# Performance work log

Hardware: AMD Instinct MI355X
Metric: run time of the kernel (lower is better)

The kernel has to match this reference:

```python
import jax, jax.numpy as jnp
import numpy as np

N, E, F_IN, HID, L, G, FFN = 100000, 1600000, 64, 128, 4, 512, 300
BN_EPS = 1e-5


def setup_inputs() -> dict:
    key = jax.random.key(0)
    ks = jax.random.split(key, 16)
    s = 0.05
    inp = {}
    inp["x"] = jax.random.normal(ks[0], (N, F_IN), dtype=jnp.float32)
    inp["edge_index"] = jax.random.randint(ks[1], (2, E), 0, N)
    inp["batch"] = jnp.sort(jax.random.randint(ks[2], (N,), 0, G))
    inp["enc_W"] = jax.random.normal(ks[3], (F_IN, HID), dtype=jnp.float32) * s
    inp["enc_b"] = jnp.zeros((HID,), jnp.float32)
    inp["Ws"] = jax.random.normal(ks[4], (L, HID, HID), dtype=jnp.float32) * s
    inp["bs"] = jnp.zeros((L, HID), jnp.float32)
    inp["bn_gamma"] = jnp.ones((L, HID), jnp.float32)
    inp["bn_beta"] = jnp.zeros((L, HID), jnp.float32)
    inp["bn_mean"] = jax.random.normal(ks[5], (L, HID), dtype=jnp.float32) * 0.01
    inp["bn_var"] = jnp.ones((L, HID), jnp.float32)
    inp["mlp_W0"] = jax.random.normal(ks[6], (HID, FFN), dtype=jnp.float32) * s
    inp["mlp_b0"] = jnp.zeros((FFN,), jnp.float32)
    inp["mlp_W1"] = jax.random.normal(ks[7], (FFN, FFN), dtype=jnp.float32) * s
    inp["mlp_b1"] = jnp.zeros((FFN,), jnp.float32)
    inp["mlp_W2"] = jax.random.normal(ks[8], (FFN, 1), dtype=jnp.float32) * s
    inp["mlp_b2"] = jnp.zeros((1,), jnp.float32)
    return inp


def reference(x, edge_index, batch, enc_W, enc_b, Ws, bs, bn_gamma, bn_beta,
              bn_mean, bn_var, mlp_W0, mlp_b0, mlp_W1, mlp_b1, mlp_W2, mlp_b2):
    # --- GCN normalization with self-loops (constant wrt params) ---
    loop = jnp.arange(N)
    row = jnp.concatenate([edge_index[0], loop])  # source
    col = jnp.concatenate([edge_index[1], loop])  # target (aggregation)
    deg = jax.ops.segment_sum(jnp.ones((E + N,), jnp.float32), col, num_segments=N)
    dinv = jnp.where(deg > 0, jax.lax.rsqrt(deg), 0.0)
    norm = dinv[row] * dinv[col]  # [E+N]

    # node encoder
    h = x @ enc_W + enc_b  # [N, HID]

    for i in range(L):
        h_prev = h
        # GCNConv: D^-1/2 (A+I) D^-1/2 (h W) + b
        hw = h @ Ws[i]
        msg = norm[:, None] * hw[row]                      # [E+N, HID]
        h = jax.ops.segment_sum(msg, col, num_segments=N) + bs[i]
        # BatchNorm1d (eval mode, running stats)
        h = (h - bn_mean[i]) * jax.lax.rsqrt(bn_var[i] + BN_EPS) * bn_gamma[i] + bn_beta[i]
        h = jax.nn.relu(h)
        if i > 0:
            h = h + h_prev

    # global mean pool over graphs
    sums = jax.ops.segment_sum(h, batch, num_segments=G)   # [G, HID]
    cnts = jax.ops.segment_sum(jnp.ones((N,), jnp.float32), batch, num_segments=G)
    gfeat = sums / jnp.maximum(cnts, 1.0)[:, None]

    # output MLP
    o = jax.nn.relu(gfeat @ mlp_W0 + mlp_b0)
    o = jax.nn.relu(o @ mlp_W1 + mlp_b1)
    return o @ mlp_W2 + mlp_b2  # [G, 1]
```

## Files before the change

kernel.cpp:

```cpp
#include <hip/hip_runtime.h>
#include <hip/hip_fp16.h>

#define NN 100000
#define NE 1600000
#define FIN 64
#define HID 128
#define NL 4
#define NG 512
#define FFN 300
#define BN_EPS 1e-5f
#define LDH 136
#define NB 512
#define NPB 196
#define CURPAD 16

static inline size_t alignup(size_t x) { return (x + 255) & ~(size_t)255; }

struct half8 { __half2 h[4]; };

typedef _Float16 f16;
typedef __attribute__((ext_vector_type(4))) _Float16 f16x4;
typedef __attribute__((ext_vector_type(8))) _Float16 f16x8;
typedef __attribute__((ext_vector_type(4))) float f32x4;

__global__ __launch_bounds__(1024) void k_bcount(const int* __restrict__ col,
                                                 int* __restrict__ bcnt) {
    __shared__ int h[NB];
    int t = threadIdx.x;
    if (t < NB) h[t] = 0;
    __syncthreads();
    for (int e = blockIdx.x * 1024 + t; e < NE; e += 256 * 1024)
        atomicAdd(&h[col[e] / NPB], 1);
    __syncthreads();
    if (t < NB && h[t] > 0) atomicAdd(&bcnt[t], h[t]);
}

__global__ void k_bscan(const int* __restrict__ bcnt, int* __restrict__ bbase,
                        int* __restrict__ bcur) {
    __shared__ int s[NB];
    int t = threadIdx.x;
    int v = bcnt[t];
    s[t] = v;
    __syncthreads();
    for (int off = 1; off < NB; off <<= 1) {
        int u = (t >= off) ? s[t - off] : 0;
        __syncthreads();
        s[t] += u;
        __syncthreads();
    }
    int excl = s[t] - v;
    bbase[t] = excl;
    bcur[t * CURPAD] = excl;
    if (t == NB - 1) bbase[NB] = s[t];
}

__global__ __launch_bounds__(1024) void k_bscatter2(const int* __restrict__ row,
                                                    const int* __restrict__ col,
                                                    int* __restrict__ bcur,
                                                    int* __restrict__ ebuf) {
    __shared__ int hcnt[NB];
    __shared__ int hbase[NB];
    int t = threadIdx.x;
    int e0 = blockIdx.x * 4096;
    if (t < NB) hcnt[t] = 0;
    __syncthreads();
    #pragma unroll
    for (int k = 0; k < 4; ++k) {
        int e = e0 + k * 1024 + t;
        if (e < NE) atomicAdd(&hcnt[col[e] / NPB], 1);
    }
    __syncthreads();
    if (t < NB) {
        int c = hcnt[t];
        hbase[t] = (c > 0) ? atomicAdd(&bcur[t * CURPAD], c) : 0;
    }
    __syncthreads();
    if (t < NB) hcnt[t] = 0;
    __syncthreads();
    #pragma unroll
    for (int k = 0; k < 4; ++k) {
        int e = e0 + k * 1024 + t;
        if (e < NE) {
            int c = col[e];
            int b = c / NPB;
            int loc = atomicAdd(&hcnt[b], 1);
            ebuf[hbase[b] + loc] = row[e] | ((c - b * NPB) << 17);
        }
    }
}

__global__ __launch_bounds__(256) void k_binfill(const int* __restrict__ ebuf,
                                                 const int* __restrict__ bbase,
                                                 int* __restrict__ offs,
                                                 int* __restrict__ ends,
                                                 float* __restrict__ dinv,
                                                 int* __restrict__ csr_src) {
    __shared__ int cnt[NPB];
    __shared__ int scn[256];
    __shared__ int cur[NPB];
    int b = blockIdx.x, t = threadIdx.x;
    int lo = b * NPB;
    int hi = lo + NPB; if (hi > NN) hi = NN;
    int n = hi - lo;
    if (n <= 0) return;
    int s0 = bbase[b], s1 = bbase[b + 1];
    for (int i = t; i < NPB; i += 256) cnt[i] = 0;
    __syncthreads();
    for (int j = s0 + t; j < s1; j += 256)
        atomicAdd(&cnt[((unsigned)ebuf[j]) >> 17], 1);
    __syncthreads();
    int v = (t < n) ? cnt[t] : 0;
    scn[t] = v;
    __syncthreads();
    for (int off = 1; off < 256; off <<= 1) {
        int u = (t >= off) ? scn[t - off] : 0;
        __syncthreads();
        scn[t] += u;
        __syncthreads();
    }
    if (t < n) {
        int g = s0 + scn[t] - v;
        offs[lo + t] = g;
        ends[lo + t] = g + v;
        dinv[lo + t] = rsqrtf((float)(v + 1));
        cur[t] = g;
    }
    __syncthreads();
    for (int j = s0 + t; j < s1; j += 256) {
        int e = ebuf[j];
        int pos = atomicAdd(&cur[((unsigned)e) >> 17], 1);
        csr_src[pos] = e & 0x1FFFF;
    }
}

__global__ void k_convW(const float* __restrict__ Ws, const float* __restrict__ encW,
                        f16* __restrict__ wt, f16* __restrict__ wte) {
    int tid = blockIdx.x * 256 + threadIdx.x;
    for (int i = tid; i < NL * HID * HID; i += 64 * 256) {
        int l = i >> 14, rem = i & 16383;
        int c = rem >> 7, k = rem & 127;
        wt[i] = (f16)Ws[(l << 14) + k * HID + c];
    }
    for (int i = tid; i < HID * FIN; i += 64 * 256) {
        int c = i >> 6, k = i & 63;
        wte[i] = (f16)encW[k * HID + c];
    }
}

__global__ __launch_bounds__(256) void k_enc_mfma(const float* __restrict__ x,
                                                  const f16* __restrict__ wte,
                                                  const float* __restrict__ b,
                                                  __half* __restrict__ h) {
    __shared__ f16 sx[64 * 72];
    __shared__ f16 sw[128 * 72];
    int t = threadIdx.x;
    int row0 = blockIdx.x * 64;
    for (int idx = t; idx < 64 * 16; idx += 256) {
        int r = idx >> 4, c4 = (idx & 15) * 4;
        float4 v = {0.0f, 0.0f, 0.0f, 0.0f};
        if (row0 + r < NN) v = *(const float4*)(x + (size_t)(row0 + r) * FIN + c4);
        f16x4 o = {(f16)v.x, (f16)v.y, (f16)v.z, (f16)v.w};
        *(f16x4*)&sx[r * 72 + c4] = o;
    }
    for (int idx = t; idx < 128 * 8; idx += 256) {
        int c = idx >> 3, ch = (idx & 7) * 8;
        *(f16x8*)&sw[c * 72 + ch] = *(const f16x8*)(wte + c * FIN + ch);
    }
    __syncthreads();
    int w = t >> 6, lane = t & 63;
    int lrow = lane & 15, lk = (lane >> 4) * 8;
    f32x4 acc[8];
    #pragma unroll
    for (int ct = 0; ct < 8; ++ct) acc[ct] = (f32x4){0.0f, 0.0f, 0.0f, 0.0f};
    const f16* pa = &sx[(w * 16 + lrow) * 72 + lk];
    #pragma unroll
    for (int ks = 0; ks < 2; ++ks) {
        f16x8 a = *(const f16x8*)(pa + ks * 32);
        #pragma unroll
        for (int ct = 0; ct < 8; ++ct) {
            f16x8 bb = *(const f16x8*)&sw[(ct * 16 + lrow) * 72 + ks * 32 + lk];
            acc[ct] = __builtin_amdgcn_mfma_f32_16x16x32_f16(a, bb, acc[ct], 0, 0, 0);
        }
    }
    float bv[8];
    #pragma unroll
    for (int ct = 0; ct < 8; ++ct) bv[ct] = b[ct * 16 + lrow];
    int rbase = row0 + w * 16 + (lane >> 4) * 4;
    #pragma unroll
    for (int i = 0; i < 4; ++i) {
        int grow = rbase + i;
        if (grow < NN) {
            #pragma unroll
            for (int ct = 0; ct < 8; ++ct)
                h[(size_t)grow * HID + ct * 16 + lrow] = __float2half(acc[ct][i] + bv[ct]);
        }
    }
}

__global__ __launch_bounds__(256) void k_gemm_mfma(const __half* __restrict__ h,
                                                   const f16* __restrict__ wt,
                                                   const float* __restrict__ dinv,
                                                   __half* __restrict__ hw) {
    __shared__ f16 sh[64 * LDH];
    __shared__ f16 sw[128 * LDH];
    int t = threadIdx.x;
    int row0 = blockIdx.x * 64;
    for (int idx = t; idx < 64 * 16; idx += 256) {
        int r = idx >> 4, ch = (idx & 15) * 8;
        f16x8 v = {0, 0, 0, 0, 0, 0, 0, 0};
        if (row0 + r < NN) v = *(const f16x8*)(h + (size_t)(row0 + r) * HID + ch);
        *(f16x8*)&sh[r * LDH + ch] = v;
    }
    for (int idx = t; idx < 128 * 16; idx += 256) {
        int c = idx >> 4, ch = (idx & 15) * 8;
        *(f16x8*)&sw[c * LDH + ch] = *(const f16x8*)(wt + c * HID + ch);
    }
    __syncthreads();
    int w = t >> 6, lane = t & 63;
    int lrow = lane & 15, lk = (lane >> 4) * 8;
    f32x4 acc[8];
    #pragma unroll
    for (int ct = 0; ct < 8; ++ct) acc[ct] = (f32x4){0.0f, 0.0f, 0.0f, 0.0f};
    const f16* pa = &sh[(w * 16 + lrow) * LDH + lk];
    #pragma unroll
    for (int ks = 0; ks < 4; ++ks) {
        f16x8 a = *(const f16x8*)(pa + ks * 32);
        #pragma unroll
        for (int ct = 0; ct < 8; ++ct) {
            f16x8 b = *(const f16x8*)&sw[(ct * 16 + lrow) * LDH + ks * 32 + lk];
            acc[ct] = __builtin_amdgcn_mfma_f32_16x16x32_f16(a, b, acc[ct], 0, 0, 0);
        }
    }
    int rbase = row0 + w * 16 + (lane >> 4) * 4;
    #pragma unroll
    for (int i = 0; i < 4; ++i) {
        int grow = rbase + i;
        if (grow < NN) {
            float dv = dinv[grow];
            #pragma unroll
            for (int ct = 0; ct < 8; ++ct)
                hw[(size_t)grow * HID + ct * 16 + lrow] = __float2half(dv * acc[ct][i]);
        }
    }
}

__device__ __forceinline__ void add8(float* a, float4 raw) {
    const __half2* p = (const __half2*)&raw;
    #pragma unroll
    for (int q = 0; q < 4; ++q) {
        float2 u = __half22float2(p[q]);
        a[2 * q] += u.x;
        a[2 * q + 1] += u.y;
    }
}

__global__ __launch_bounds__(256) void k_gather(
    const int* __restrict__ offs, const int* __restrict__ ends,
    const int* __restrict__ csr_src,
    const float* __restrict__ dinv,
    const __half* __restrict__ hw, const __half* __restrict__ hprev,
    const float* __restrict__ bias, const float* __restrict__ gamma,
    const float* __restrict__ beta, const float* __restrict__ mean,
    const float* __restrict__ var,
    __half* __restrict__ hout, int with_res) {
    int node = (blockIdx.x * 256 + threadIdx.x) >> 6;
    if (node >= NN) return;
    int lane = threadIdx.x & 63;
    int grp = lane >> 4;
    int fb = (lane & 15) * 8;
    int s = offs[node], e = ends[node];
    float a[8] = {0, 0, 0, 0, 0, 0, 0, 0};
    int j = s + grp;
    for (; j + 12 < e; j += 16) {
        int s0 = csr_src[j], s1 = csr_src[j + 4], s2 = csr_src[j + 8], s3 = csr_src[j + 12];
        float4 r0 = *(const float4*)(hw + (size_t)s0 * HID + fb);
        float4 r1 = *(const float4*)(hw + (size_t)s1 * HID + fb);
        float4 r2 = *(const float4*)(hw + (size_t)s2 * HID + fb);
        float4 r3 = *(const float4*)(hw + (size_t)s3 * HID + fb);
        add8(a, r0); add8(a, r1); add8(a, r2); add8(a, r3);
    }
    for (; j + 4 < e; j += 8) {
        int s0 = csr_src[j], s1 = csr_src[j + 4];
        float4 r0 = *(const float4*)(hw + (size_t)s0 * HID + fb);
        float4 r1 = *(const float4*)(hw + (size_t)s1 * HID + fb);
        add8(a, r0); add8(a, r1);
    }
    for (; j < e; j += 4) {
        int s0 = csr_src[j];
        float4 r0 = *(const float4*)(hw + (size_t)s0 * HID + fb);
        add8(a, r0);
    }
    #pragma unroll
    for (int q = 0; q < 8; ++q) {
        a[q] += __shfl_xor(a[q], 16);
        a[q] += __shfl_xor(a[q], 32);
    }
    if (grp) return;
    float4 sraw = *(const float4*)(hw + (size_t)node * HID + fb);
    add8(a, sraw);
    float dc = dinv[node];
    float4 bi0 = *(const float4*)(bias + fb),  bi1 = *(const float4*)(bias + fb + 4);
    float4 mn0 = *(const float4*)(mean + fb),  mn1 = *(const float4*)(mean + fb + 4);
    float4 vr0 = *(const float4*)(var + fb),   vr1 = *(const float4*)(var + fb + 4);
    float4 gm0 = *(const float4*)(gamma + fb), gm1 = *(const float4*)(gamma + fb + 4);
    float4 bt0 = *(const float4*)(beta + fb),  bt1 = *(const float4*)(beta + fb + 4);
    float bi[8] = {bi0.x, bi0.y, bi0.z, bi0.w, bi1.x, bi1.y, bi1.z, bi1.w};
    float mn[8] = {mn0.x, mn0.y, mn0.z, mn0.w, mn1.x, mn1.y, mn1.z, mn1.w};
    float vr[8] = {vr0.x, vr0.y, vr0.z, vr0.w, vr1.x, vr1.y, vr1.z, vr1.w};
    float gm[8] = {gm0.x, gm0.y, gm0.z, gm0.w, gm1.x, gm1.y, gm1.z, gm1.w};
    float bt[8] = {bt0.x, bt0.y, bt0.z, bt0.w, bt1.x, bt1.y, bt1.z, bt1.w};
    float o[8];
    #pragma unroll
    for (int q = 0; q < 8; ++q)
        o[q] = fmaxf((dc * a[q] + bi[q] - mn[q]) * rsqrtf(vr[q] + BN_EPS) * gm[q] + bt[q], 0.0f);
    if (with_res) {
        float4 praw = *(const float4*)(hprev + (size_t)node * HID + fb);
        const __half2* pp = (const __half2*)&praw;
        #pragma unroll
        for (int q = 0; q < 4; ++q) {
            float2 p = __half22float2(pp[q]);
            o[2 * q] += p.x;
            o[2 * q + 1] += p.y;
        }
    }
    half8 ov;
    #pragma unroll
    for (int q = 0; q < 4; ++q)
        ov.h[q] = __floats2half2_rn(o[2 * q], o[2 * q + 1]);
    *(half8*)(hout + (size_t)node * HID + fb) = ov;
}

__device__ __forceinline__ int lower_bound_dev(const int* __restrict__ a, int n, int v) {
    int lo = 0, hi = n;
    while (lo < hi) {
        int m = (lo + hi) >> 1;
        if (a[m] < v) lo = m + 1; else hi = m;
    }
    return lo;
}

__global__ __launch_bounds__(256) void k_pool_seg(const __half* __restrict__ h,
                                                  const int* __restrict__ batch,
                                                  float* __restrict__ gfeat) {
    __shared__ int range[2];
    __shared__ float s[256];
    int g = blockIdx.x, t = threadIdx.x;
    if (t == 0) {
        range[0] = lower_bound_dev(batch, NN, g);
        range[1] = lower_bound_dev(batch, NN, g + 1);
    }
    __syncthreads();
    int start = range[0], end = range[1];
    int f = t & 127, half = t >> 7;
    float acc = 0.0f;
    for (int i = start + half; i < end; i += 2)
        acc += __half2float(h[(size_t)i * HID + f]);
    s[t] = acc;
    __syncthreads();
    if (t < 128) {
        float sum = s[t] + s[t + 128];
        float cnt = (float)(end - start);
        gfeat[(size_t)g * HID + t] = sum / fmaxf(cnt, 1.0f);
    }
}

__global__ void k_mlp0(const float* __restrict__ gfeat,
                       const float* __restrict__ W, const float* __restrict__ b,
                       float* __restrict__ out) {
    __shared__ float srow[HID];
    int g = blockIdx.x, t = threadIdx.x;
    if (t < HID) srow[t] = gfeat[(size_t)g * HID + t];
    __syncthreads();
    for (int j = t; j < FFN; j += 128) {
        float acc = b[j];
        for (int k = 0; k < HID; ++k) acc += srow[k] * W[k * FFN + j];
        out[(size_t)g * FFN + j] = fmaxf(acc, 0.0f);
    }
}

__global__ void k_mlp1(const float* __restrict__ in, const float* __restrict__ W,
                       const float* __restrict__ b, float* __restrict__ out) {
    __shared__ float srow[FFN];
    int g = blockIdx.x, t = threadIdx.x;
    for (int k = t; k < FFN; k += 128) srow[k] = in[(size_t)g * FFN + k];
    __syncthreads();
    for (int j = t; j < FFN; j += 128) {
        float acc = b[j];
        for (int k = 0; k < FFN; ++k) acc += srow[k] * W[k * FFN + j];
        out[(size_t)g * FFN + j] = fmaxf(acc, 0.0f);
    }
}

__global__ void k_mlp2(const float* __restrict__ in, const float* __restrict__ W,
                       const float* __restrict__ b, float* __restrict__ out) {
    int g = blockIdx.x, lane = threadIdx.x;
    float acc = 0.0f;
    for (int k = lane; k < FFN; k += 64) acc += in[(size_t)g * FFN + k] * W[k];
    for (int off = 32; off > 0; off >>= 1) acc += __shfl_down(acc, off);
    if (lane == 0) out[g] = acc + b[0];
}

extern "C" void kernel_launch(void* const* d_in, const int* in_sizes, int n_in,
                              void* d_out, int out_size, void* d_ws, size_t ws_size,
                              hipStream_t stream) {
    const float* x    = (const float*)d_in[0];
    const int*   ei   = (const int*)d_in[1];
    const int*   batch= (const int*)d_in[2];
    const float* encW = (const float*)d_in[3];
    const float* encb = (const float*)d_in[4];
    const float* Ws   = (const float*)d_in[5];
    const float* bs   = (const float*)d_in[6];
    const float* gam  = (const float*)d_in[7];
    const float* bet  = (const float*)d_in[8];
    const float* mean = (const float*)d_in[9];
    const float* var  = (const float*)d_in[10];
    const float* W0   = (const float*)d_in[11];
    const float* b0   = (const float*)d_in[12];
    const float* W1   = (const float*)d_in[13];
    const float* b1   = (const float*)d_in[14];
    const float* W2   = (const float*)d_in[15];
    const float* b2   = (const float*)d_in[16];
    float* out = (float*)d_out;

    char* w = (char*)d_ws;
    float*  dinv    = (float*)w;  w += alignup((size_t)NN * 4);
    int*    offs    = (int*)w;    w += alignup((size_t)NN * 4);
    int*    ends    = (int*)w;    w += alignup((size_t)NN * 4);
    int*    csr_src = (int*)w;    w += alignup((size_t)NE * 4);
    int*    bcnt    = (int*)w;    w += alignup((size_t)NB * 4);
    int*    bbase   = (int*)w;    w += alignup((size_t)(NB + 1) * 4);
    int*    bcur    = (int*)w;    w += alignup((size_t)NB * CURPAD * 4);
    int*    ebuf    = (int*)w;    w += alignup((size_t)NE * 4);
    __half* hA      = (__half*)w; w += alignup((size_t)NN * HID * 2);
    __half* hB      = (__half*)w; w += alignup((size_t)NN * HID * 2);
    __half* hw_     = (__half*)w; w += alignup((size_t)NN * HID * 2);
    f16*    wt      = (f16*)w;    w += alignup((size_t)NL * HID * HID * 2);
    f16*    wte     = (f16*)w;    w += alignup((size_t)HID * FIN * 2);
    float*  gfeat   = (float*)w;  w += alignup((size_t)NG * HID * 4);
    float*  m0      = (float*)w;  w += alignup((size_t)NG * FFN * 4);
    float*  m1      = (float*)w;  w += alignup((size_t)NG * FFN * 4);

    const int* row = ei;
    const int* col = ei + NE;

    hipMemsetAsync(bcnt, 0, (size_t)NB * 4, stream);
    k_bcount<<<256, 1024, 0, stream>>>(col, bcnt);
    k_bscan<<<1, NB, 0, stream>>>(bcnt, bbase, bcur);
    k_bscatter2<<<(NE + 4095) / 4096, 1024, 0, stream>>>(row, col, bcur, ebuf);
    k_binfill<<<NB, 256, 0, stream>>>(ebuf, bbase, offs, ends, dinv, csr_src);

    k_convW<<<64, 256, 0, stream>>>(Ws, encW, wt, wte);
    k_enc_mfma<<<(NN + 63) / 64, 256, 0, stream>>>(x, wte, encb, hA);

    __half* hcur = hA;
    __half* hnext = hB;
    for (int l = 0; l < NL; ++l) {
        k_gemm_mfma<<<(NN + 63) / 64, 256, 0, stream>>>(hcur, wt + (size_t)l * HID * HID, dinv, hw_);
        k_gather<<<(NN * 64 + 255) / 256, 256, 0, stream>>>(
            offs, ends, csr_src, dinv, hw_, hcur,
            bs + l * HID, gam + l * HID, bet + l * HID, mean + l * HID, var + l * HID,
            hnext, l > 0 ? 1 : 0);
        __half* tmp = hcur; hcur = hnext; hnext = tmp;
    }

    k_pool_seg<<<NG, 256, 0, stream>>>(hcur, batch, gfeat);
    k_mlp0<<<NG, 128, 0, stream>>>(gfeat, W0, b0, m0);
    k_mlp1<<<NG, 128, 0, stream>>>(m0, W1, b1, m1);
    k_mlp2<<<NG, 64, 0, stream>>>(m1, W2, b2, out);
}
```

Measured before the change: 523.9 us.

## Split features into 16-channel slabs so gather works per-slab for cache locality

Stores hidden activations in a channel-partitioned layout (8 slabs of 16 features, each node row 32 bytes), so each gather block handles one slab for 16 nodes. The intent is that each slab (about 3.2 MB) stays resident in L2 while the random neighbor gathers run, instead of scattering 256-byte rows across the whole 25 MB tensor. In exchange, each neighbor access fetches only 32 bytes, CSR indices are re-read 8 times, and every lane loads a half2 instead of 16 bytes. The GEMM, encoder and pooling kernels are adapted to read and write the new layout.

```diff
diff --git a/kernel.cpp b/kernel.cpp
--- a/kernel.cpp
+++ b/kernel.cpp
@@ -13,6 +13,8 @@
 #define NB 512
 #define NPB 196
 #define CURPAD 16
+#define NCH 8
+#define CH 16
 
 static inline size_t alignup(size_t x) { return (x + 255) & ~(size_t)255; }
 
@@ -150,7 +152,7 @@
 __global__ __launch_bounds__(256) void k_enc_mfma(const float* __restrict__ x,
                                                   const f16* __restrict__ wte,
                                                   const float* __restrict__ b,
-                                                  __half* __restrict__ h) {
+                                                  __half* __restrict__ hc) {
     __shared__ f16 sx[64 * 72];
     __shared__ f16 sw[128 * 72];
     int t = threadIdx.x;
@@ -192,24 +194,27 @@
         if (grow < NN) {
             #pragma unroll
             for (int ct = 0; ct < 8; ++ct)
-                h[(size_t)grow * HID + ct * 16 + lrow] = __float2half(acc[ct][i] + bv[ct]);
-        }
-    }
-}
-
-__global__ __launch_bounds__(256) void k_gemm_mfma(const __half* __restrict__ h,
+                hc[((size_t)ct * NN + grow) * CH + lrow] = __float2half(acc[ct][i] + bv[ct]);
+        }
+    }
+}
+
+__global__ __launch_bounds__(256) void k_gemm_mfma(const __half* __restrict__ hcin,
                                                    const f16* __restrict__ wt,
                                                    const float* __restrict__ dinv,
-                                                   __half* __restrict__ hw) {
+                                                   __half* __restrict__ hwc) {
     __shared__ f16 sh[64 * LDH];
     __shared__ f16 sw[128 * LDH];
     int t = threadIdx.x;
     int row0 = blockIdx.x * 64;
-    for (int idx = t; idx < 64 * 16; idx += 256) {
-        int r = idx >> 4, ch = (idx & 15) * 8;
+    for (int idx = t; idx < 1024; idx += 256) {
+        int cc = idx >> 7;
+        int l = idx & 127;
+        int r = l >> 1, half = l & 1;
         f16x8 v = {0, 0, 0, 0, 0, 0, 0, 0};
-        if (row0 + r < NN) v = *(const f16x8*)(h + (size_t)(row0 + r) * HID + ch);
-        *(f16x8*)&sh[r * LDH + ch] = v;
+        if (row0 + r < NN)
+            v = *(const f16x8*)(hcin + ((size_t)cc * NN + row0 + r) * CH + half * 8);
+        *(f16x8*)&sh[r * LDH + cc * 16 + half * 8] = v;
     }
     for (int idx = t; idx < 128 * 16; idx += 256) {
         int c = idx >> 4, ch = (idx & 15) * 8;
@@ -239,95 +244,74 @@
             float dv = dinv[grow];
             #pragma unroll
             for (int ct = 0; ct < 8; ++ct)
-                hw[(size_t)grow * HID + ct * 16 + lrow] = __float2half(dv * acc[ct][i]);
-        }
-    }
-}
-
-__device__ __forceinline__ void add8(float* a, float4 raw) {
-    const __half2* p = (const __half2*)&raw;
-    #pragma unroll
-    for (int q = 0; q < 4; ++q) {
-        float2 u = __half22float2(p[q]);
-        a[2 * q] += u.x;
-        a[2 * q + 1] += u.y;
-    }
-}
-
-__global__ __launch_bounds__(256) void k_gather(
+                hwc[((size_t)ct * NN + grow) * CH + lrow] = __float2half(dv * acc[ct][i]);
+        }
+    }
+}
+
+__global__ __launch_bounds__(256) void k_gather_cp(
     const int* __restrict__ offs, const int* __restrict__ ends,
     const int* __restrict__ csr_src,
     const float* __restrict__ dinv,
-    const __half* __restrict__ hw, const __half* __restrict__ hprev,
+    const __half* __restrict__ hwc, const __half* __restrict__ hprevc,
     const float* __restrict__ bias, const float* __restrict__ gamma,
     const float* __restrict__ beta, const float* __restrict__ mean,
     const float* __restrict__ var,
-    __half* __restrict__ hout, int with_res) {
-    int node = (blockIdx.x * 256 + threadIdx.x) >> 6;
-    if (node >= NN) return;
-    int lane = threadIdx.x & 63;
-    int grp = lane >> 4;
-    int fb = (lane & 15) * 8;
-    int s = offs[node], e = ends[node];
-    float a[8] = {0, 0, 0, 0, 0, 0, 0, 0};
-    int j = s + grp;
-    for (; j + 12 < e; j += 16) {
-        int s0 = csr_src[j], s1 = csr_src[j + 4], s2 = csr_src[j + 8], s3 = csr_src[j + 12];
-        float4 r0 = *(const float4*)(hw + (size_t)s0 * HID + fb);
-        float4 r1 = *(const float4*)(hw + (size_t)s1 * HID + fb);
-        float4 r2 = *(const float4*)(hw + (size_t)s2 * HID + fb);
-        float4 r3 = *(const float4*)(hw + (size_t)s3 * HID + fb);
-        add8(a, r0); add8(a, r1); add8(a, r2); add8(a, r3);
-    }
-    for (; j + 4 < e; j += 8) {
-        int s0 = csr_src[j], s1 = csr_src[j + 4];
-        float4 r0 = *(const float4*)(hw + (size_t)s0 * HID + fb);
-        float4 r1 = *(const float4*)(hw + (size_t)s1 * HID + fb);
-        add8(a, r0); add8(a, r1);
-    }
-    for (; j < e; j += 4) {
-        int s0 = csr_src[j];
-        float4 r0 = *(const float4*)(hw + (size_t)s0 * HID + fb);
-        add8(a, r0);
-    }
-    #pragma unroll
-    for (int q = 0; q < 8; ++q) {
-        a[q] += __shfl_xor(a[q], 16);
-        a[q] += __shfl_xor(a[q], 32);
-    }
-    if (grp) return;
-    float4 sraw = *(const float4*)(hw + (size_t)node * HID + fb);
-    add8(a, sraw);
-    float dc = dinv[node];
-    float4 bi0 = *(const float4*)(bias + fb),  bi1 = *(const float4*)(bias + fb + 4);
-    float4 mn0 = *(const float4*)(mean + fb),  mn1 = *(const float4*)(mean + fb + 4);
-    float4 vr0 = *(const float4*)(var + fb),   vr1 = *(const float4*)(var + fb + 4);
-    float4 gm0 = *(const float4*)(gamma + fb), gm1 = *(const float4*)(gamma + fb + 4);
-    float4 bt0 = *(const float4*)(beta + fb),  bt1 = *(const float4*)(beta + fb + 4);
-    float bi[8] = {bi0.x, bi0.y, bi0.z, bi0.w, bi1.x, bi1.y, bi1.z, bi1.w};
-    float mn[8] = {mn0.x, mn0.y, mn0.z, mn0.w, mn1.x, mn1.y, mn1.z, mn1.w};
-    float vr[8] = {vr0.x, vr0.y, vr0.z, vr0.w, vr1.x, vr1.y, vr1.z, vr1.w};
-    float gm[8] = {gm0.x, gm0.y, gm0.z, gm0.w, gm1.x, gm1.y, gm1.z, gm1.w};
-    float bt[8] = {bt0.x, bt0.y, bt0.z, bt0.w, bt1.x, bt1.y, bt1.z, bt1.w};
-    float o[8];
-    #pragma unroll
-    for (int q = 0; q < 8; ++q)
-        o[q] = fmaxf((dc * a[q] + bi[q] - mn[q]) * rsqrtf(vr[q] + BN_EPS) * gm[q] + bt[q], 0.0f);
-    if (with_res) {
-        float4 praw = *(const float4*)(hprev + (size_t)node * HID + fb);
-        const __half2* pp = (const __half2*)&praw;
-        #pragma unroll
-        for (int q = 0; q < 4; ++q) {
-            float2 p = __half22float2(pp[q]);
-            o[2 * q] += p.x;
-            o[2 * q + 1] += p.y;
-        }
-    }
-    half8 ov;
-    #pragma unroll
-    for (int q = 0; q < 4; ++q)
-        ov.h[q] = __floats2half2_rn(o[2 * q], o[2 * q + 1]);
-    *(half8*)(hout + (size_t)node * HID + fb) = ov;
+    __half* __restrict__ houtc, int with_res) {
+    int bid = blockIdx.x;
+    int c = bid & 7;
+    int nb = bid >> 3;
+    int w = threadIdx.x >> 6, lane = threadIdx.x & 63;
+    int g = lane >> 3, fl = lane & 7;
+    const __half* slab = hwc + (size_t)c * NN * CH;
+    int f0 = c * CH + fl * 2;
+    float2 bi = *(const float2*)(bias + f0);
+    float2 mn = *(const float2*)(mean + f0);
+    float2 vr = *(const float2*)(var + f0);
+    float2 gm = *(const float2*)(gamma + f0);
+    float2 bt = *(const float2*)(beta + f0);
+    float rs0 = rsqrtf(vr.x + BN_EPS) * gm.x;
+    float rs1 = rsqrtf(vr.y + BN_EPS) * gm.y;
+    #pragma unroll
+    for (int it = 0; it < 4; ++it) {
+        int node = nb * 16 + w * 4 + it;
+        if (node >= NN) break;
+        int s = offs[node], e = ends[node];
+        float a0 = 0.0f, a1 = 0.0f;
+        int j = s + g;
+        for (; j + 8 < e; j += 16) {
+            int s0 = csr_src[j], s1 = csr_src[j + 8];
+            float2 v0 = __half22float2(*(const __half2*)(slab + (size_t)s0 * CH + fl * 2));
+            float2 v1 = __half22float2(*(const __half2*)(slab + (size_t)s1 * CH + fl * 2));
+            a0 += v0.x + v1.x;
+            a1 += v0.y + v1.y;
+        }
+        for (; j < e; j += 8) {
+            int s0 = csr_src[j];
+            float2 v0 = __half22float2(*(const __half2*)(slab + (size_t)s0 * CH + fl * 2));
+            a0 += v0.x;
+            a1 += v0.y;
+        }
+        a0 += __shfl_xor(a0, 8);  a1 += __shfl_xor(a1, 8);
+        a0 += __shfl_xor(a0, 16); a1 += __shfl_xor(a1, 16);
+        a0 += __shfl_xor(a0, 32); a1 += __shfl_xor(a1, 32);
+        if (g == 0) {
+            float2 hv = __half22float2(*(const __half2*)(slab + (size_t)node * CH + fl * 2));
+            float dc = dinv[node];
+            a0 = dc * (a0 + hv.x);
+            a1 = dc * (a1 + hv.y);
+            float o0 = fmaxf((a0 + bi.x - mn.x) * rs0 + bt.x, 0.0f);
+            float o1 = fmaxf((a1 + bi.y - mn.y) * rs1 + bt.y, 0.0f);
+            if (with_res) {
+                float2 p = __half22float2(
+                    *(const __half2*)(hprevc + ((size_t)c * NN + node) * CH + fl * 2));
+                o0 += p.x;
+                o1 += p.y;
+            }
+            *(__half2*)(houtc + ((size_t)c * NN + node) * CH + fl * 2) =
+                __floats2half2_rn(o0, o1);
+        }
+    }
 }
 
 __device__ __forceinline__ int lower_bound_dev(const int* __restrict__ a, int n, int v) {
@@ -339,7 +323,7 @@
     return lo;
 }
 
-__global__ __launch_bounds__(256) void k_pool_seg(const __half* __restrict__ h,
+__global__ __launch_bounds__(256) void k_pool_seg(const __half* __restrict__ hc,
                                                   const int* __restrict__ batch,
                                                   float* __restrict__ gfeat) {
     __shared__ int range[2];
@@ -352,9 +336,11 @@
     __syncthreads();
     int start = range[0], end = range[1];
     int f = t & 127, half = t >> 7;
+    int cf = f >> 4, fl = f & 15;
+    const __half* slab = hc + (size_t)cf * NN * CH;
     float acc = 0.0f;
     for (int i = start + half; i < end; i += 2)
-        acc += __half2float(h[(size_t)i * HID + f]);
+        acc += __half2float(slab[(size_t)i * CH + fl]);
     s[t] = acc;
     __syncthreads();
     if (t < 128) {
@@ -456,7 +442,7 @@
     __half* hnext = hB;
     for (int l = 0; l < NL; ++l) {
         k_gemm_mfma<<<(NN + 63) / 64, 256, 0, stream>>>(hcur, wt + (size_t)l * HID * HID, dinv, hw_);
-        k_gather<<<(NN * 64 + 255) / 256, 256, 0, stream>>>(
+        k_gather_cp<<<(NN / 16) * NCH, 256, 0, stream>>>(
             offs, ends, csr_src, dinv, hw_, hcur,
             bs + l * HID, gam + l * HID, bet + l * HID, mean + l * HID, var + l * HID,
             hnext, l > 0 ? 1 : 0);
```

Result: slower. 1.087 ms (+107.6%).

## Split node features into two 64-channel slabs for cache-friendly gather

Applied to the files above, without the earlier changes.

Node feature buffers are stored as two channel slabs of 64 halves each ([2][N][64]) instead of [N][128]. The gather kernel launches twice as many blocks, with even and odd blocks each aggregating one slab, and every wave uses 8 edge groups of 8 lanes. Each slab of hw is half the size, so the randomly gathered working set is more likely to stay in L2/MALL. In exchange, csr_src and offsets are read twice, each gather moves only 128 bytes per row, and the encoder, GEMM and pool kernels must use the strided slab indexing.

```diff
diff --git a/kernel.cpp b/kernel.cpp
--- a/kernel.cpp
+++ b/kernel.cpp
@@ -13,6 +13,7 @@
 #define NB 512
 #define NPB 196
 #define CURPAD 16
+#define CH2 64
 
 static inline size_t alignup(size_t x) { return (x + 255) & ~(size_t)255; }
 
@@ -150,7 +151,7 @@
 __global__ __launch_bounds__(256) void k_enc_mfma(const float* __restrict__ x,
                                                   const f16* __restrict__ wte,
                                                   const float* __restrict__ b,
-                                                  __half* __restrict__ h) {
+                                                  __half* __restrict__ hc) {
     __shared__ f16 sx[64 * 72];
     __shared__ f16 sw[128 * 72];
     int t = threadIdx.x;
@@ -192,24 +193,26 @@
         if (grow < NN) {
             #pragma unroll
             for (int ct = 0; ct < 8; ++ct)
-                h[(size_t)grow * HID + ct * 16 + lrow] = __float2half(acc[ct][i] + bv[ct]);
-        }
-    }
-}
-
-__global__ __launch_bounds__(256) void k_gemm_mfma(const __half* __restrict__ h,
+                hc[((size_t)(ct >> 2) * NN + grow) * CH2 + (ct & 3) * 16 + lrow] =
+                    __float2half(acc[ct][i] + bv[ct]);
+        }
+    }
+}
+
+__global__ __launch_bounds__(256) void k_gemm_mfma(const __half* __restrict__ hcin,
                                                    const f16* __restrict__ wt,
                                                    const float* __restrict__ dinv,
-                                                   __half* __restrict__ hw) {
+                                                   __half* __restrict__ hwc) {
     __shared__ f16 sh[64 * LDH];
     __shared__ f16 sw[128 * LDH];
     int t = threadIdx.x;
     int row0 = blockIdx.x * 64;
-    for (int idx = t; idx < 64 * 16; idx += 256) {
-        int r = idx >> 4, ch = (idx & 15) * 8;
+    for (int idx = t; idx < 1024; idx += 256) {
+        int r = idx >> 4, u = idx & 15;
         f16x8 v = {0, 0, 0, 0, 0, 0, 0, 0};
-        if (row0 + r < NN) v = *(const f16x8*)(h + (size_t)(row0 + r) * HID + ch);
-        *(f16x8*)&sh[r * LDH + ch] = v;
+        if (row0 + r < NN)
+            v = *(const f16x8*)(hcin + ((size_t)(u >> 3) * NN + row0 + r) * CH2 + (u & 7) * 8);
+        *(f16x8*)&sh[r * LDH + u * 8] = v;
     }
     for (int idx = t; idx < 128 * 16; idx += 256) {
         int c = idx >> 4, ch = (idx & 15) * 8;
@@ -239,7 +242,8 @@
             float dv = dinv[grow];
             #pragma unroll
             for (int ct = 0; ct < 8; ++ct)
-                hw[(size_t)grow * HID + ct * 16 + lrow] = __float2half(dv * acc[ct][i]);
+                hwc[((size_t)(ct >> 2) * NN + grow) * CH2 + (ct & 3) * 16 + lrow] =
+                    __float2half(dv * acc[ct][i]);
         }
     }
 }
@@ -254,56 +258,54 @@
     }
 }
 
-__global__ __launch_bounds__(256) void k_gather(
+__global__ __launch_bounds__(256) void k_gather_c2(
     const int* __restrict__ offs, const int* __restrict__ ends,
     const int* __restrict__ csr_src,
     const float* __restrict__ dinv,
-    const __half* __restrict__ hw, const __half* __restrict__ hprev,
+    const __half* __restrict__ hwc, const __half* __restrict__ hprevc,
     const float* __restrict__ bias, const float* __restrict__ gamma,
     const float* __restrict__ beta, const float* __restrict__ mean,
     const float* __restrict__ var,
-    __half* __restrict__ hout, int with_res) {
-    int node = (blockIdx.x * 256 + threadIdx.x) >> 6;
+    __half* __restrict__ houtc, int with_res) {
+    int bid = blockIdx.x;
+    int c = bid & 1;
+    int node = ((bid >> 1) * 256 + (int)threadIdx.x) >> 6;
     if (node >= NN) return;
     int lane = threadIdx.x & 63;
-    int grp = lane >> 4;
-    int fb = (lane & 15) * 8;
+    int g = lane >> 3;
+    int fb = (lane & 7) * 8;
+    const __half* slab = hwc + (size_t)c * NN * CH2;
     int s = offs[node], e = ends[node];
     float a[8] = {0, 0, 0, 0, 0, 0, 0, 0};
-    int j = s + grp;
-    for (; j + 12 < e; j += 16) {
-        int s0 = csr_src[j], s1 = csr_src[j + 4], s2 = csr_src[j + 8], s3 = csr_src[j + 12];
-        float4 r0 = *(const float4*)(hw + (size_t)s0 * HID + fb);
-        float4 r1 = *(const float4*)(hw + (size_t)s1 * HID + fb);
-        float4 r2 = *(const float4*)(hw + (size_t)s2 * HID + fb);
-        float4 r3 = *(const float4*)(hw + (size_t)s3 * HID + fb);
-        add8(a, r0); add8(a, r1); add8(a, r2); add8(a, r3);
-    }
-    for (; j + 4 < e; j += 8) {
-        int s0 = csr_src[j], s1 = csr_src[j + 4];
-        float4 r0 = *(const float4*)(hw + (size_t)s0 * HID + fb);
-        float4 r1 = *(const float4*)(hw + (size_t)s1 * HID + fb);
-        add8(a, r0); add8(a, r1);
-    }
-    for (; j < e; j += 4) {
+    int j = s + g;
+    for (; j + 8 < e; j += 16) {
+        int s0 = csr_src[j], s1 = csr_src[j + 8];
+        float4 r0 = *(const float4*)(slab + (size_t)s0 * CH2 + fb);
+        float4 r1 = *(const float4*)(slab + (size_t)s1 * CH2 + fb);
+        add8(a, r0);
+        add8(a, r1);
+    }
+    for (; j < e; j += 8) {
         int s0 = csr_src[j];
-        float4 r0 = *(const float4*)(hw + (size_t)s0 * HID + fb);
+        float4 r0 = *(const float4*)(slab + (size_t)s0 * CH2 + fb);
         add8(a, r0);
     }
     #pragma unroll
     for (int q = 0; q < 8; ++q) {
+        a[q] += __shfl_xor(a[q], 8);
         a[q] += __shfl_xor(a[q], 16);
         a[q] += __shfl_xor(a[q], 32);
     }
-    if (grp) return;
-    float4 sraw = *(const float4*)(hw + (size_t)node * HID + fb);
+    if (g) return;
+    float4 sraw = *(const float4*)(slab + (size_t)node * CH2 + fb);
     add8(a, sraw);
     float dc = dinv[node];
-    float4 bi0 = *(const float4*)(bias + fb),  bi1 = *(const float4*)(bias + fb + 4);
-    float4 mn0 = *(const float4*)(mean + fb),  mn1 = *(const float4*)(mean + fb + 4);
-    float4 vr0 = *(const float4*)(var + fb),   vr1 = *(const float4*)(var + fb + 4);
-    float4 gm0 = *(const float4*)(gamma + fb), gm1 = *(const float4*)(gamma + fb + 4);
-    float4 bt0 = *(const float4*)(beta + fb),  bt1 = *(const float4*)(beta + fb + 4);
+    int f0 = c * CH2 + fb;
+    float4 bi0 = *(const float4*)(bias + f0),  bi1 = *(const float4*)(bias + f0 + 4);
+    float4 mn0 = *(const float4*)(mean + f0),  mn1 = *(const float4*)(mean + f0 + 4);
+    float4 vr0 = *(const float4*)(var + f0),   vr1 = *(const float4*)(var + f0 + 4);
+    float4 gm0 = *(const float4*)(gamma + f0), gm1 = *(const float4*)(gamma + f0 + 4);
+    float4 bt0 = *(const float4*)(beta + f0),  bt1 = *(const float4*)(beta + f0 + 4);
     float bi[8] = {bi0.x, bi0.y, bi0.z, bi0.w, bi1.x, bi1.y, bi1.z, bi1.w};
     float mn[8] = {mn0.x, mn0.y, mn0.z, mn0.w, mn1.x, mn1.y, mn1.z, mn1.w};
     float vr[8] = {vr0.x, vr0.y, vr0.z, vr0.w, vr1.x, vr1.y, vr1.z, vr1.w};
@@ -314,7 +316,7 @@
     for (int q = 0; q < 8; ++q)
         o[q] = fmaxf((dc * a[q] + bi[q] - mn[q]) * rsqrtf(vr[q] + BN_EPS) * gm[q] + bt[q], 0.0f);
     if (with_res) {
-        float4 praw = *(const float4*)(hprev + (size_t)node * HID + fb);
+        float4 praw = *(const float4*)(hprevc + ((size_t)c * NN + node) * CH2 + fb);
         const __half2* pp = (const __half2*)&praw;
         #pragma unroll
         for (int q = 0; q < 4; ++q) {
@@ -327,7 +329,7 @@
     #pragma unroll
     for (int q = 0; q < 4; ++q)
         ov.h[q] = __floats2half2_rn(o[2 * q], o[2 * q + 1]);
-    *(half8*)(hout + (size_t)node * HID + fb) = ov;
+    *(half8*)(houtc + ((size_t)c * NN + node) * CH2 + fb) = ov;
 }
 
 __device__ __forceinline__ int lower_bound_dev(const int* __restrict__ a, int n, int v) {
@@ -339,7 +341,7 @@
     return lo;
 }
 
-__global__ __launch_bounds__(256) void k_pool_seg(const __half* __restrict__ h,
+__global__ __launch_bounds__(256) void k_pool_seg(const __half* __restrict__ hc,
                                                   const int* __restrict__ batch,
                                                   float* __restrict__ gfeat) {
     __shared__ int range[2];
@@ -352,9 +354,11 @@
     __syncthreads();
     int start = range[0], end = range[1];
     int f = t & 127, half = t >> 7;
+    const __half* slab = hc + (size_t)(f >> 6) * NN * CH2;
+    int fl = f & 63;
     float acc = 0.0f;
     for (int i = start + half; i < end; i += 2)
-        acc += __half2float(h[(size_t)i * HID + f]);
+        acc += __half2float(slab[(size_t)i * CH2 + fl]);
     s[t] = acc;
     __syncthreads();
     if (t < 128) {
@@ -456,7 +460,7 @@
     __half* hnext = hB;
     for (int l = 0; l < NL; ++l) {
         k_gemm_mfma<<<(NN + 63) / 64, 256, 0, stream>>>(hcur, wt + (size_t)l * HID * HID, dinv, hw_);
-        k_gather<<<(NN * 64 + 255) / 256, 256, 0, stream>>>(
+        k_gather_c2<<<2 * ((NN * 64 + 255) / 256), 256, 0, stream>>>(
             offs, ends, csr_src, dinv, hw_, hcur,
             bs + l * HID, gam + l * HID, bet + l * HID, mean + l * HID, var + l * HID,
             hnext, l > 0 ? 1 : 0);
```

New measurement: 686.7 us. 31.1% more time.
